# Kernel optimization log

Measured on AMD Instinct MI355X. Metric: run time of the kernel, lower is better.

The kernel has to match this reference:

```python
import jax, jax.numpy as jnp
import numpy as np

B, CIN, COUT, H, W = 4, 64, 64, 192, 192
KS, N, EPS = 3, 9, 1e-5


def setup_inputs() -> dict:
    key = jax.random.key(0)
    ks = jax.random.split(key, 4)
    return {
        "inputs": jax.random.normal(ks[0], (B, CIN, H, W), jnp.float32),
        "w_p": jax.random.normal(ks[1], (2 * N, CIN, KS, KS), jnp.float32) * 0.01,
        "b_p": jnp.zeros((2 * N,), jnp.float32),
        "w_m": jax.random.normal(ks[2], (N, CIN, KS, KS), jnp.float32) * 0.05,
        "b_m": jnp.zeros((N,), jnp.float32),
        "w_conv": jax.random.normal(ks[3], (COUT, CIN, KS, KS), jnp.float32) * (1.0 / np.sqrt(CIN * N)),
        "gamma": jnp.ones((COUT,), jnp.float32),
        "beta": jnp.zeros((COUT,), jnp.float32),
    }


def _conv3x3(x, w, b):
    y = jax.lax.conv_general_dilated(x, w, (1, 1), ((1, 1), (1, 1)),
                                     dimension_numbers=("NCHW", "OIHW", "NCHW"))
    return y + b[None, :, None, None]


def reference(inputs, w_p, b_p, w_m, b_m, w_conv, gamma, beta):
    x = inputs
    b, c, h, w = x.shape
    offset = _conv3x3(x, w_p, b_p)                 # (B, 2N, H, W)
    m = jax.nn.sigmoid(_conv3x3(x, w_m, b_m))      # (B, N, H, W)

    xp = jnp.pad(x, ((0, 0), (0, 0), (1, 1), (1, 1)))  # zero pad by 1
    hp, wp = h + 2, w + 2

    off = offset.transpose(0, 2, 3, 1)             # (B, H, W, 2N), first N=y, last N=x
    ky, kx = jnp.meshgrid(jnp.arange(-1, 2), jnp.arange(-1, 2), indexing="ij")
    pny = ky.reshape(-1).astype(x.dtype)           # (N,) kernel dy, ky-major order
    pnx = kx.reshape(-1).astype(x.dtype)
    p0y = jnp.arange(1, h + 1, dtype=x.dtype)      # base coords in padded image
    p0x = jnp.arange(1, w + 1, dtype=x.dtype)

    py = p0y[None, :, None, None] + pny + off[..., :N]   # (B, H, W, N)
    px = p0x[None, None, :, None] + pnx + off[..., N:]

    qy0 = jnp.clip(jnp.floor(py), 0, hp - 1)
    qy1 = jnp.clip(jnp.floor(py) + 1, 0, hp - 1)
    qx0 = jnp.clip(jnp.floor(px), 0, wp - 1)
    qx1 = jnp.clip(jnp.floor(px) + 1, 0, wp - 1)
    pyc = jnp.clip(py, 0, hp - 1)
    pxc = jnp.clip(px, 0, wp - 1)

    g_lt = (1 + (qy0 - pyc)) * (1 + (qx0 - pxc))
    g_rb = (1 - (qy1 - pyc)) * (1 - (qx1 - pxc))
    g_lb = (1 + (qy0 - pyc)) * (1 - (qx1 - pxc))
    g_rt = (1 - (qy1 - pyc)) * (1 + (qx0 - pxc))

    xf = xp.reshape(b, c, hp * wp)

    def gather(qy, qx):
        idx = (qy.astype(jnp.int32) * wp + qx.astype(jnp.int32)).reshape(b, 1, -1)
        idx = jnp.broadcast_to(idx, (b, c, idx.shape[-1]))
        return jnp.take_along_axis(xf, idx, axis=2).reshape(b, c, h, w, N)

    x_s = (g_lt[:, None] * gather(qy0, qx0)
           + g_rb[:, None] * gather(qy1, qx1)
           + g_lb[:, None] * gather(qy0, qx1)
           + g_rt[:, None] * gather(qy1, qx0))          # (B, C, H, W, N)
    x_s = x_s * m.transpose(0, 2, 3, 1)[:, None]        # modulation (B,1,H,W,N)

    # main conv over the 9 sampled taps (== conv with stride=ks on rearranged tensor)
    out = jnp.einsum("bchwn,ocn->bohw", x_s, w_conv.reshape(w_conv.shape[0], c, N))

    # BatchNorm2d (training mode: batch stats), ReLU, MaxPool(2)
    mu = out.mean((0, 2, 3), keepdims=True)
    var = ((out - mu) ** 2).mean((0, 2, 3), keepdims=True)
    out = gamma[None, :, None, None] * (out - mu) * jax.lax.rsqrt(var + EPS) + beta[None, :, None, None]
    out = jax.nn.relu(out)
    bo, co, ho, wo = out.shape
    out = out.reshape(bo, co, ho // 2, 2, wo // 2, 2).max(axis=(3, 5))
    return out
```

## Files before the change

### kernel.cpp

```cpp
#include <hip/hip_runtime.h>
#include <hip/hip_bf16.h>
#include <math.h>

#define HW     192
#define PLANE  (HW*HW)
#define CIN    64
#define COUT   64
#define NB     4
#define NPIX   (NB*PLANE)
#define H2     194
#define W2     200
#define WR     7
#define WC     21
#define NPOS   (WR*WC)

typedef __attribute__((ext_vector_type(8))) short bf16x8;
typedef __attribute__((ext_vector_type(4))) float f32x4;
typedef __attribute__((ext_vector_type(2))) float f32x2;

static __device__ __forceinline__ ushort f2bf(float f) {
    __hip_bfloat16 h = __float2bfloat16(f);
    return __builtin_bit_cast(ushort, h);
}
static __device__ __forceinline__ float bf2f(ushort u) {
    return __builtin_bit_cast(float, ((unsigned)u) << 16);
}
static __device__ __forceinline__ f32x2 up2(unsigned u) {
    f32x2 r;
    r.x = __builtin_bit_cast(float, u << 16);
    r.y = __builtin_bit_cast(float, u & 0xffff0000u);
    return r;
}

__global__ __launch_bounds__(256) void kpadprep(
    const float* __restrict__ x,
    const float* __restrict__ wc, const float* __restrict__ w_p,
    const float* __restrict__ w_m,
    ushort* __restrict__ xt, ushort* __restrict__ wbf, ushort* __restrict__ womf)
{
    int blk = blockIdx.x;
    int t   = threadIdx.x;
    if (blk < NB * H2 * 2) {
        __shared__ ushort sT[100 * 72];
        int half = blk & 1;
        int y    = (blk >> 1) % H2;
        int b    = (blk >> 1) / H2;
        int col0 = half * 100;
        const float* xb = x + (size_t)b * CIN * PLANE;
        bool yok = (y >= 1 && y <= HW);
#pragma unroll
        for (int it = 0; it < 13; ++it) {
            int idx = t + 256 * it;
            if (idx < 3200) {
                int cp   = (idx * 5243) >> 19;
                int lcol = idx - cp * 100;
                int col  = col0 + lcol;
                int c    = cp * 2;
                float v0 = 0.f, v1 = 0.f;
                if (yok && col >= 1 && col <= HW) {
                    const float* s0 = xb + (size_t)c * PLANE + (y - 1) * HW + (col - 1);
                    v0 = s0[0]; v1 = s0[PLANE];
                }
                *(unsigned*)&sT[lcol * 72 + c] =
                    (unsigned)f2bf(v0) | ((unsigned)f2bf(v1) << 16);
            }
        }
        __syncthreads();
        uint4* dst = (uint4*)(xt + ((size_t)(b * H2 + y) * W2) * 64);
#pragma unroll
        for (int it = 0; it < 4; ++it) {
            int idx = t + 256 * it;
            if (idx < 800) {
                int lcol = idx >> 3, g = idx & 7;
                dst[(col0 + lcol) * 8 + g] = *(uint4*)&sT[lcol * 72 + g * 8];
            }
        }
        return;
    }
    int i = (blk - NB * H2 * 2) * 256 + t;
    if (i < 4608) {
        int lane  = i & 63;
        int rc    = i >> 6;
        int chunk = rc % 18;
        int og    = rc / 18;
        int o  = og * 16 + (lane & 15);
        int k0 = chunk * 32 + (lane >> 4) * 8;
        ushort v[8];
#pragma unroll
        for (int j = 0; j < 8; ++j) {
            int k = k0 + j, c = k & 63, n = k >> 6;
            v[j] = f2bf(wc[o * 576 + c * 9 + n]);
        }
        ((uint4*)wbf)[i] = *(uint4*)v;
    } else if (i < 6912) {
        int ii    = i - 4608;
        int lane  = ii & 63;
        int rc    = ii >> 6;
        int chunk = rc % 18;
        int og    = rc / 18;
        int co = og * 16 + (lane & 15);
        int k0 = chunk * 32 + (lane >> 4) * 8;
        ushort v[8];
#pragma unroll
        for (int j = 0; j < 8; ++j) {
            int k = k0 + j, c = k & 63, n = k >> 6;
            float w = 0.f;
            if (co < 18)      w = w_p[(co * 64 + c) * 9 + n];
            else if (co < 27) w = w_m[((co - 18) * 64 + c) * 9 + n];
            v[j] = f2bf(w);
        }
        ((uint4*)womf)[ii] = *(uint4*)v;
    }
}

__global__ __launch_bounds__(256, 4) void kdeform(
    const ushort* __restrict__ xt,
    const ushort* __restrict__ wbf, const ushort* __restrict__ womf,
    const float* __restrict__ b_p, const float* __restrict__ b_m,
    ushort* __restrict__ outp)
{
    __shared__ __align__(16) char smem[40708];
    ushort* sWin = (ushort*)smem;
    ushort* sXF  = (ushort*)(smem + 18816);
    float (*sOM)[17] = (float(*)[17])(smem + 18816);
    float4 (*sG)[16] = (float4(*)[16])(smem + 37248);
    uint (*sPos)[16] = (uint(*)[16])(smem + 39552);
    uint (*sOg)[16]  = (uint(*)[16])(smem + 40128);
    int* sFlag = (int*)(smem + 40704);

    int t    = threadIdx.x;
    int pix0 = blockIdx.x * 16;
    int b    = pix0 / PLANE;
    int rem  = pix0 - b * PLANE;
    int h    = rem / HW;
    int w0   = rem - h * HW;
    int rbase = min(max(h - 2, 0), H2 - WR);
    int wbase = min(max(w0 - 2, 0), W2 - WC - 4);
    if (t == 0) *sFlag = 0;

    const ushort* xtb = xt + (size_t)(b * H2) * W2 * 64;

    {
        const uint4* gsrc = (const uint4*)(xtb + ((size_t)rbase * W2 + wbase) * 64);
#pragma unroll
        for (int it = 0; it < 5; ++it) {
            int idx = t + 256 * it;
            if (idx < NPOS * 8) {
                int pos = idx >> 3, s = idx & 7;
                int g   = (s - pos) & 7;
                int r   = (pos * 3121) >> 16;
                int cc  = pos - r * WC;
                *(uint4*)&sWin[pos * 64 + s * 8] = gsrc[((r * W2 + cc) << 3) + g];
            }
        }
    }
    __syncthreads();

    if (t < 128) {
        int lane = t & 63, og = t >> 6;
        int sub  = lane >> 4;
        int hr   = h - rbase;
        int wrp  = w0 - wbase + (lane & 15);
        f32x4 acc = {0.f, 0.f, 0.f, 0.f};
#pragma unroll
        for (int chunk = 0; chunk < 18; ++chunk) {
            bf16x8 a = *(const bf16x8*)&womf[((og * 18 + chunk) * 64 + lane) * 8];
            int n  = chunk >> 1;
            int dy = n / 3, dx = n - dy * 3;
            int pos  = (hr + dy) * WC + wrp + dx;
            int slot = ((chunk & 1) * 4 + sub + pos) & 7;
            bf16x8 bb = *(const bf16x8*)&sWin[pos * 64 + slot * 8];
            acc = __builtin_amdgcn_mfma_f32_16x16x32_bf16(a, bb, acc, 0, 0, 0);
        }
        int col = lane & 15, row0 = sub * 4;
#pragma unroll
        for (int r = 0; r < 4; ++r) sOM[og * 16 + row0 + r][col] = acc[r];
    }
    __syncthreads();

    uint pkC = 0, ogC = 0; float4 gC;
    if (t < 144) {
        int pp = t & 15, n = t >> 4;
        float offy = sOM[n][pp]      + b_p[n];
        float offx = sOM[9 + n][pp]  + b_p[9 + n];
        float mr   = sOM[18 + n][pp] + b_m[n];
        float m = 1.f / (1.f + __expf(-mr));
        int dy = n / 3, dx = n - dy * 3;
        float py = (float)(h + dy) + offy;
        float px = (float)(w0 + pp + dx) + offx;
        float fy = floorf(py), fx = floorf(px);
        float qy0 = fminf(fmaxf(fy,       0.f), 193.f);
        float qy1 = fminf(fmaxf(fy + 1.f, 0.f), 193.f);
        float qx0 = fminf(fmaxf(fx,       0.f), 193.f);
        float qx1 = fminf(fmaxf(fx + 1.f, 0.f), 193.f);
        float pyc = fminf(fmaxf(py, 0.f), 193.f);
        float pxc = fminf(fmaxf(px, 0.f), 193.f);
        float ay = 1.f + qy0 - pyc, by = 1.f - (qy1 - pyc);
        float ax = 1.f + qx0 - pxc, bx = 1.f - (qx1 - pxc);
        int ry0 = (int)qy0, ry1 = (int)qy1;
        int cx0 = (int)qx0, cx1 = (int)qx1;
        int xs  = cx1 - cx0;
        ogC = (uint)(ry0 | (ry1 << 8) | (cx0 << 16) | (xs << 24));
        int p00 = (ry0 - rbase) * WC + (cx0 - wbase);
        int p10 = (ry1 - rbase) * WC + (cx0 - wbase);
        pkC = (uint)((p00 & 255) | (((p00 + xs) & 255) << 8)
                   | ((p10 & 255) << 16) | (((p10 + xs) & 255) << 24));
        gC = make_float4(ay * ax * m, ay * bx * m, by * ax * m, by * bx * m);
        if (ry0 < rbase || ry1 > rbase + (WR - 1) ||
            cx0 < wbase || cx1 > wbase + (WC - 1))
            atomicOr(sFlag, 1);
    }
    __syncthreads();
    if (t < 144) {
        int pp = t & 15, n = t >> 4;
        sOg[n][pp]  = ogC;
        sPos[n][pp] = pkC;
        sG[n][pp]   = gC;
    }
    __syncthreads();

    {
        int px  = t & 15, sub = t >> 4;
        int o8  = sub & 7;
        bool fb = (*sFlag != 0);
#pragma unroll
        for (int it = 0; it < 5; ++it) {
            int item = sub + 16 * it;
            if (item >= 72) break;
            int n = item >> 3;
            float4 G = sG[n][px];
            uint4 A0, A1, C0, C1;
            if (!fb) {
                uint pk = sPos[n][px];
                int p00 = pk & 255, p01 = (pk >> 8) & 255;
                int p10 = (pk >> 16) & 255, p11 = pk >> 24;
                A0 = *(const uint4*)&sWin[p00 * 64 + ((o8 + p00) & 7) * 8];
                A1 = *(const uint4*)&sWin[p01 * 64 + ((o8 + p01) & 7) * 8];
                C0 = *(const uint4*)&sWin[p10 * 64 + ((o8 + p10) & 7) * 8];
                C1 = *(const uint4*)&sWin[p11 * 64 + ((o8 + p11) & 7) * 8];
            } else {
                uint gp = sOg[n][px];
                int ry0 = gp & 255, ry1 = (gp >> 8) & 255;
                int cx0 = (gp >> 16) & 255, xs = gp >> 24;
                const ushort* g0 = xtb + (size_t)(ry0 * W2 + cx0) * 64 + o8 * 8;
                const ushort* g1 = xtb + (size_t)(ry1 * W2 + cx0) * 64 + o8 * 8;
                A0 = *(const uint4*)g0;
                A1 = *(const uint4*)(g0 + xs * 64);
                C0 = *(const uint4*)g1;
                C1 = *(const uint4*)(g1 + xs * 64);
            }
            unsigned ua0[4] = {A0.x, A0.y, A0.z, A0.w};
            unsigned ua1[4] = {A1.x, A1.y, A1.z, A1.w};
            unsigned uc0[4] = {C0.x, C0.y, C0.z, C0.w};
            unsigned uc1[4] = {C1.x, C1.y, C1.z, C1.w};
            ushort pk8[8] __attribute__((aligned(16)));
#pragma unroll
            for (int q = 0; q < 4; ++q) {
                f32x2 v = G.x * up2(ua0[q]) + G.y * up2(ua1[q])
                        + G.z * up2(uc0[q]) + G.w * up2(uc1[q]);
                pk8[2 * q]     = f2bf(v.x);
                pk8[2 * q + 1] = f2bf(v.y);
            }
            int chunk = n * 2 + (o8 >> 2), s16 = o8 & 3;
            *(uint4*)&sXF[(chunk * 64 + s16 * 16 + (px ^ s16)) * 8] = *(uint4*)pk8;
        }
    }
    __syncthreads();

    {
        int lane = t & 63, og = t >> 6;
        int sub = lane >> 4, pcol = lane & 15;
        f32x4 acc = {0.f, 0.f, 0.f, 0.f};
#pragma unroll
        for (int chunk = 0; chunk < 18; ++chunk) {
            bf16x8 a  = *(const bf16x8*)&wbf[((og * 18 + chunk) * 64 + lane) * 8];
            bf16x8 bb = *(const bf16x8*)&sXF[(chunk * 64 + sub * 16 + (pcol ^ sub)) * 8];
            acc = __builtin_amdgcn_mfma_f32_16x16x32_bf16(a, bb, acc, 0, 0, 0);
        }
        int row0 = sub * 4;
        ushort* ob = outp + ((size_t)(b * COUT + og * 16 + row0)) * PLANE + rem + pcol;
        ob[0]                 = f2bf(acc[0]);
        ob[(size_t)PLANE]     = f2bf(acc[1]);
        ob[2 * (size_t)PLANE] = f2bf(acc[2]);
        ob[3 * (size_t)PLANE] = f2bf(acc[3]);
    }
}

__global__ __launch_bounds__(256) void kstats(
    const ushort* __restrict__ outp, float* __restrict__ partial)
{
    int o  = blockIdx.x >> 3;
    int sl = blockIdx.x & 7;
    int t  = threadIdx.x;
    float s = 0.f, s2 = 0.f;
    for (int b = 0; b < NB; ++b) {
        const uint4* pl = (const uint4*)(outp + ((size_t)(b * COUT + o)) * PLANE
                                         + sl * (PLANE / 8));
        for (int i = t; i < PLANE / 64; i += 256) {
            uint4 v = pl[i];
            unsigned ua[4] = {v.x, v.y, v.z, v.w};
#pragma unroll
            for (int j = 0; j < 4; ++j) {
                float lo = __builtin_bit_cast(float, ua[j] << 16);
                float hi = __builtin_bit_cast(float, ua[j] & 0xffff0000u);
                s  += lo + hi;
                s2 += lo * lo + hi * hi;
            }
        }
    }
    __shared__ float rs[256], rs2[256];
    rs[t] = s; rs2[t] = s2;
    __syncthreads();
    for (int st = 128; st > 0; st >>= 1) {
        if (t < st) { rs[t] += rs[t + st]; rs2[t] += rs2[t + st]; }
        __syncthreads();
    }
    if (t == 0) {
        partial[o * 8 + sl]       = rs[0];
        partial[512 + o * 8 + sl] = rs2[0];
    }
}

__global__ __launch_bounds__(256) void kbnpool(
    const ushort* __restrict__ outp, const float* __restrict__ partial,
    const float* __restrict__ gamma, const float* __restrict__ beta,
    float* __restrict__ out)
{
    int i = blockIdx.x * 256 + threadIdx.x;
    int wo  = i % 96;
    int tmp = i / 96;
    int ho  = tmp % 96; tmp /= 96;
    int o   = tmp % 64;
    int b   = tmp / 64;
    float s = 0.f, s2 = 0.f;
#pragma unroll
    for (int sl = 0; sl < 8; ++sl) {
        s  += partial[o * 8 + sl];
        s2 += partial[512 + o * 8 + sl];
    }
    float inv  = 1.f / (float)(NB * PLANE);
    float mean = s * inv;
    float var  = s2 * inv - mean * mean;
    float rsq  = rsqrtf(var + 1e-5f);
    float g  = gamma[o] * rsq;
    float bt = beta[o] - mean * g;
    const ushort* pl = outp + ((size_t)(b * COUT + o)) * PLANE + (2 * ho) * HW + 2 * wo;
    unsigned u01 = *(const unsigned*)pl;
    unsigned u23 = *(const unsigned*)(pl + HW);
    float y00 = fmaxf(g * bf2f((ushort)(u01 & 0xffff)) + bt, 0.f);
    float y01 = fmaxf(g * bf2f((ushort)(u01 >> 16))    + bt, 0.f);
    float y10 = fmaxf(g * bf2f((ushort)(u23 & 0xffff)) + bt, 0.f);
    float y11 = fmaxf(g * bf2f((ushort)(u23 >> 16))    + bt, 0.f);
    out[i] = fmaxf(fmaxf(y00, y01), fmaxf(y10, y11));
}

extern "C" void kernel_launch(void* const* d_in, const int* in_sizes, int n_in,
                              void* d_out, int out_size, void* d_ws, size_t ws_size,
                              hipStream_t stream)
{
    const float* x      = (const float*)d_in[0];
    const float* w_p    = (const float*)d_in[1];
    const float* b_p    = (const float*)d_in[2];
    const float* w_m    = (const float*)d_in[3];
    const float* b_m    = (const float*)d_in[4];
    const float* w_conv = (const float*)d_in[5];
    const float* gamma  = (const float*)d_in[6];
    const float* beta   = (const float*)d_in[7];
    float* out = (float*)d_out;

    char* ws = (char*)d_ws;
    ushort* xt      = (ushort*)ws;
    ushort* outp    = (ushort*)(ws + 19865600);
    float*  partial = (float*)(ws + 38739968);
    ushort* wbf     = (ushort*)(ws + 38744064);
    ushort* womf    = (ushort*)(ws + 38817792);

    kpadprep<<<NB * H2 * 2 + 27, 256, 0, stream>>>(x, w_conv, w_p, w_m, xt, wbf, womf);
    kdeform<<<NPIX / 16, 256, 0, stream>>>(xt, wbf, womf, b_p, b_m, outp);
    kstats<<<512, 256, 0, stream>>>(outp, partial);
    kbnpool<<<(NB * COUT * 96 * 96) / 256, 256, 0, stream>>>(outp, partial, gamma, beta, out);
}
```

Baseline: 181.9 us.

## Vectorize pad-transpose prep and split offset/mask MFMA across all four waves

The padding/transposition prep kernel now handles a full padded row per block, reading input with float4 loads and zeroing only the border columns explicitly, which halves the block count and widens global loads. In the deformable kernel the offset/modulation MFMA reduction over 18 chunks is split between two wave pairs (9 chunks each) so all four waves participate, writing two partial tiles to shared memory that are summed when computing sampling coordinates. This shortens the serial MFMA chain per block at the cost of extra shared-memory space and reads, and the larger prep shared tile may reduce occupancy.

```diff
diff --git a/kernel.cpp b/kernel.cpp
--- a/kernel.cpp
+++ b/kernel.cpp
@@ -40,44 +40,47 @@
 {
     int blk = blockIdx.x;
     int t   = threadIdx.x;
-    if (blk < NB * H2 * 2) {
-        __shared__ ushort sT[100 * 72];
-        int half = blk & 1;
-        int y    = (blk >> 1) % H2;
-        int b    = (blk >> 1) / H2;
-        int col0 = half * 100;
-        const float* xb = x + (size_t)b * CIN * PLANE;
+    if (blk < NB * H2) {
+        __shared__ ushort sT[W2 * 72];
+        int b = blk / H2, y = blk % H2;
         bool yok = (y >= 1 && y <= HW);
-#pragma unroll
-        for (int it = 0; it < 13; ++it) {
+        const float* xb = x + (size_t)b * CIN * PLANE + (size_t)(y - 1) * HW;
+        {
+            int zi  = t >> 5;
+            int col = (zi == 0) ? 0 : 192 + zi;
+            *(unsigned*)&sT[col * 72 + (t & 31) * 2] = 0;
+        }
+#pragma unroll
+        for (int it = 0; it < 6; ++it) {
             int idx = t + 256 * it;
-            if (idx < 3200) {
-                int cp   = (idx * 5243) >> 19;
-                int lcol = idx - cp * 100;
-                int col  = col0 + lcol;
-                int c    = cp * 2;
-                float v0 = 0.f, v1 = 0.f;
-                if (yok && col >= 1 && col <= HW) {
-                    const float* s0 = xb + (size_t)c * PLANE + (y - 1) * HW + (col - 1);
-                    v0 = s0[0]; v1 = s0[PLANE];
-                }
-                *(unsigned*)&sT[lcol * 72 + c] =
-                    (unsigned)f2bf(v0) | ((unsigned)f2bf(v1) << 16);
-            }
+            int cp  = idx / 48;
+            int q   = idx - cp * 48;
+            int c   = cp * 2;
+            float4 v0 = make_float4(0.f, 0.f, 0.f, 0.f), v1 = v0;
+            if (yok) {
+                v0 = *(const float4*)(xb + (size_t)c * PLANE + 4 * q);
+                v1 = *(const float4*)(xb + (size_t)(c + 1) * PLANE + 4 * q);
+            }
+            float a0[4] = {v0.x, v0.y, v0.z, v0.w};
+            float a1[4] = {v1.x, v1.y, v1.z, v1.w};
+#pragma unroll
+            for (int j = 0; j < 4; ++j)
+                *(unsigned*)&sT[(4 * q + 1 + j) * 72 + c] =
+                    (unsigned)f2bf(a0[j]) | ((unsigned)f2bf(a1[j]) << 16);
         }
         __syncthreads();
         uint4* dst = (uint4*)(xt + ((size_t)(b * H2 + y) * W2) * 64);
 #pragma unroll
-        for (int it = 0; it < 4; ++it) {
+        for (int it = 0; it < 7; ++it) {
             int idx = t + 256 * it;
-            if (idx < 800) {
-                int lcol = idx >> 3, g = idx & 7;
-                dst[(col0 + lcol) * 8 + g] = *(uint4*)&sT[lcol * 72 + g * 8];
+            if (idx < 1600) {
+                int col = idx >> 3, g = idx & 7;
+                dst[col * 8 + g] = *(uint4*)&sT[col * 72 + g * 8];
             }
         }
         return;
     }
-    int i = (blk - NB * H2 * 2) * 256 + t;
+    int i = (blk - NB * H2) * 256 + t;
     if (i < 4608) {
         int lane  = i & 63;
         int rc    = i >> 6;
@@ -122,7 +125,8 @@
     __shared__ __align__(16) char smem[40708];
     ushort* sWin = (ushort*)smem;
     ushort* sXF  = (ushort*)(smem + 18816);
-    float (*sOM)[17] = (float(*)[17])(smem + 18816);
+    float (*sOMa)[17] = (float(*)[17])(smem + 18816);
+    float (*sOMb)[17] = (float(*)[17])(smem + 18816 + 2176);
     float4 (*sG)[16] = (float4(*)[16])(smem + 37248);
     uint (*sPos)[16] = (uint(*)[16])(smem + 39552);
     uint (*sOg)[16]  = (uint(*)[16])(smem + 40128);
@@ -156,14 +160,18 @@
     }
     __syncthreads();
 
-    if (t < 128) {
-        int lane = t & 63, og = t >> 6;
+    {
+        int lane = t & 63;
+        int wv   = t >> 6;
+        int og   = wv & 1;
+        int half = wv >> 1;
         int sub  = lane >> 4;
         int hr   = h - rbase;
         int wrp  = w0 - wbase + (lane & 15);
         f32x4 acc = {0.f, 0.f, 0.f, 0.f};
 #pragma unroll
-        for (int chunk = 0; chunk < 18; ++chunk) {
+        for (int cc = 0; cc < 9; ++cc) {
+            int chunk = half * 9 + cc;
             bf16x8 a = *(const bf16x8*)&womf[((og * 18 + chunk) * 64 + lane) * 8];
             int n  = chunk >> 1;
             int dy = n / 3, dx = n - dy * 3;
@@ -173,17 +181,18 @@
             acc = __builtin_amdgcn_mfma_f32_16x16x32_bf16(a, bb, acc, 0, 0, 0);
         }
         int col = lane & 15, row0 = sub * 4;
-#pragma unroll
-        for (int r = 0; r < 4; ++r) sOM[og * 16 + row0 + r][col] = acc[r];
-    }
-    __syncthreads();
-
-    uint pkC = 0, ogC = 0; float4 gC;
+        float (*dst)[17] = half ? sOMb : sOMa;
+#pragma unroll
+        for (int r = 0; r < 4; ++r) dst[og * 16 + row0 + r][col] = acc[r];
+    }
+    __syncthreads();
+
+    uint pkC = 0, ogC = 0; float4 gC = make_float4(0.f, 0.f, 0.f, 0.f);
     if (t < 144) {
         int pp = t & 15, n = t >> 4;
-        float offy = sOM[n][pp]      + b_p[n];
-        float offx = sOM[9 + n][pp]  + b_p[9 + n];
-        float mr   = sOM[18 + n][pp] + b_m[n];
+        float offy = sOMa[n][pp]      + sOMb[n][pp]      + b_p[n];
+        float offx = sOMa[9 + n][pp]  + sOMb[9 + n][pp]  + b_p[9 + n];
+        float mr   = sOMa[18 + n][pp] + sOMb[18 + n][pp] + b_m[n];
         float m = 1.f / (1.f + __expf(-mr));
         int dy = n / 3, dx = n - dy * 3;
         float py = (float)(h + dy) + offy;
@@ -375,7 +384,7 @@
     ushort* wbf     = (ushort*)(ws + 38744064);
     ushort* womf    = (ushort*)(ws + 38817792);
 
-    kpadprep<<<NB * H2 * 2 + 27, 256, 0, stream>>>(x, w_conv, w_p, w_m, xt, wbf, womf);
+    kpadprep<<<NB * H2 + 27, 256, 0, stream>>>(x, w_conv, w_p, w_m, xt, wbf, womf);
     kdeform<<<NPIX / 16, 256, 0, stream>>>(xt, wbf, womf, b_p, b_m, outp);
     kstats<<<512, 256, 0, stream>>>(outp, partial);
     kbnpool<<<(NB * COUT * 96 * 96) / 256, 256, 0, stream>>>(outp, partial, gamma, beta, out);
```

Measured after the change: 180.3 us. Within noise of the previous version (-0.9%).
